# Performance work log

Measured on AMD Instinct MI355X. Metric: run time of the kernel, lower is better.

Reference implementation:

```python
import jax, jax.numpy as jnp
import numpy as np


def ray_sampler(cam2world, intrinsics, resolution):
    # EG3D RaySampler: pixel centers in [0,1], lifted through intrinsics, rotated to world.
    B = cam2world.shape[0]
    fx = intrinsics[:, 0, 0][:, None]
    fy = intrinsics[:, 1, 1][:, None]
    cx = intrinsics[:, 0, 2][:, None]
    cy = intrinsics[:, 1, 2][:, None]
    sk = intrinsics[:, 0, 1][:, None]
    ii, jj = jnp.meshgrid(jnp.arange(resolution), jnp.arange(resolution), indexing='ij')
    # torch.meshgrid + flip(0): x = column index, y = row index (row-major flatten)
    x = ((jj.reshape(-1).astype(jnp.float32) + 0.5) / resolution)[None, :]  # [1, M]
    y = ((ii.reshape(-1).astype(jnp.float32) + 0.5) / resolution)[None, :]  # [1, M]
    x_lift = (x - cx + cy * sk / fy - sk * y / fy) / fx        # [B, M]
    y_lift = (y - cy) / fy                                     # [B, M]
    ones = jnp.ones_like(x_lift)
    cam_rel = jnp.stack([x_lift, y_lift, ones, ones], axis=-1)  # [B, M, 4]
    world = jnp.einsum('bij,bmj->bmi', cam2world, cam_rel)[..., :3]  # [B, M, 3]
    cam_loc = cam2world[:, :3, 3]                               # [B, 3]
    dirs = world - cam_loc[:, None, :]
    dirs = dirs / jnp.maximum(jnp.linalg.norm(dirs, axis=-1, keepdims=True), 1e-12)
    origins = jnp.broadcast_to(cam_loc[:, None, :], dirs.shape)
    return origins, dirs


def setup_inputs() -> dict:
    key = jax.random.key(0)
    k1, k2, k3 = jax.random.split(key, 3)
    B, res, N = 4, 128, 2048
    # realistic camera: identity rotation, camera near z=2.7 (EG3D radius), normalized intrinsics
    t = jnp.concatenate([0.05 * jax.random.normal(k1, (B, 2)), jnp.full((B, 1), 2.7)], axis=1)
    c2w = jnp.tile(jnp.eye(4, dtype=jnp.float32)[None], (B, 1, 1)).at[:, :3, 3].set(t)
    intr = jnp.tile(jnp.array([[4.2647, 0.0, 0.5], [0.0, 4.2647, 0.5], [0.0, 0.0, 1.0]],
                              dtype=jnp.float32)[None], (B, 1, 1))
    c = jnp.concatenate([c2w.reshape(B, 16), intr.reshape(B, 9)], axis=1)  # [B, 25]
    image_depth = 2.2 + jax.random.uniform(k2, (B, 1, res, res), dtype=jnp.float32)
    pc = 0.3 * jax.random.normal(k3, (B, N, 3), dtype=jnp.float32)
    return {"c": c, "image_depth": image_depth, "pc": pc, "neural_rendering_resolution": 128}


def reference(c, image_depth, pc, neural_rendering_resolution):
    B = c.shape[0]
    res = neural_rendering_resolution
    M = res * res
    cam2world = c[:, :16].reshape(B, 4, 4)
    intrinsics = c[:, 16:25].reshape(B, 3, 3)
    ray_origins, ray_dirs = ray_sampler(cam2world, intrinsics, res)  # [B, M, 3] each
    pc3 = pc[..., :3]                                                # [B, N, 3]
    # distance from camera origin to every pc point -> max per sample
    d0 = jnp.linalg.norm(ray_origins[:, :1, :] - pc3, axis=-1)       # [B, N]
    max_distance = jnp.max(d0, axis=1)                               # [B]
    depth = image_depth.reshape(B, M, 1)
    pred = depth * ray_dirs + ray_origins                            # [B, M, 3]
    mask = depth.reshape(B, M) < max_distance[:, None]               # [B, M]
    # chamfer dist1 (direction=0): squared distance of each pred point to nearest pc point
    d2 = (jnp.sum(pred * pred, axis=-1)[:, :, None]
          + jnp.sum(pc3 * pc3, axis=-1)[:, None, :]
          - 2.0 * jnp.einsum('bmd,bnd->bmn', pred, pc3))             # [B, M, N]
    min_d2 = jnp.maximum(jnp.min(d2, axis=2), 0.0)                   # [B, M]
    # ragged masked mean == mean over pred_[mask_] in the original loop
    m = mask.astype(min_d2.dtype)
    loss = jnp.sum(min_d2 * m, axis=1) / jnp.maximum(jnp.sum(m, axis=1), 1.0)
    return loss.reshape(B, 1)
```

## Files before the change

kernel.cpp:

```cpp
#include <hip/hip_runtime.h>
#include <math.h>

#define TPB 512
#define WAVES 8
#define RAYS_PB 256
#define MAXPTS 2048
#define PTILE 32

typedef short short8 __attribute__((ext_vector_type(8)));
typedef float f32x16 __attribute__((ext_vector_type(16)));

__device__ __forceinline__ unsigned int f2bf(float f) {
    unsigned int u = __float_as_uint(f);
    u += 0x7FFFu + ((u >> 16) & 1u);
    return u >> 16;
}

__global__ __launch_bounds__(TPB) void chamfer_main(
    const float* __restrict__ c, const float* __restrict__ depth,
    const float* __restrict__ pc, float2* __restrict__ partial,
    int res, int M, int N)
{
    __shared__ uint2 spts[MAXPTS];
    __shared__ float redR[WAVES][32][33];
    __shared__ float pnL[RAYS_PB], depL[RAYS_PB];
    __shared__ float smax[WAVES];
    __shared__ float bs[4], bc[4];

    int tile = blockIdx.x, b = blockIdx.y;
    int tid = threadIdx.x, w = tid >> 6, lane = tid & 63;
    int colb = lane & 31, hh = lane >> 5;

    const float* cb = c + b * 25;
    float fx = cb[16], sk = cb[17], cx = cb[18];
    float fy = cb[20], cy = cb[21];
    float ox = cb[3], oy = cb[7], oz = cb[11];

    short8 afrag = {0, 0, 0, 0, 0, 0, 0, 0};
    {
        int m = tile * RAYS_PB + w * 32 + colb;
        int mm = min(m, M - 1);
        int i = mm / res, j = mm - i * res;
        float x = (j + 0.5f) / (float)res;
        float y = (i + 0.5f) / (float)res;
        float xl = (x - cx + cy * sk / fy - sk * y / fy) / fx;
        float yl = (y - cy) / fy;
        float wx = cb[0] * xl + cb[1] * yl + cb[2] + cb[3];
        float wy = cb[4] * xl + cb[5] * yl + cb[6] + cb[7];
        float wz = cb[8] * xl + cb[9] * yl + cb[10] + cb[11];
        float dx = wx - ox, dy = wy - oy, dz = wz - oz;
        float nrm = fmaxf(sqrtf(dx * dx + dy * dy + dz * dz), 1e-12f);
        dx /= nrm; dy /= nrm; dz /= nrm;
        float d = depth[(size_t)b * M + mm];
        float px_ = fmaf(d, dx, ox);
        float py_ = fmaf(d, dy, oy);
        float pz_ = fmaf(d, dz, oz);
        float pn_ = px_ * px_ + py_ * py_ + pz_ * pz_;
        if (hh == 0) {
            pnL[w * 32 + colb] = pn_;
            depL[w * 32 + colb] = d;
            afrag[0] = (short)f2bf(px_);
            afrag[1] = (short)f2bf(py_);
            afrag[2] = (short)f2bf(pz_);
            afrag[3] = (short)0x3F80;
        }
    }

    const f32x16 zacc = {0.f,0.f,0.f,0.f,0.f,0.f,0.f,0.f,
                         0.f,0.f,0.f,0.f,0.f,0.f,0.f,0.f};
    float mx[16];
    #pragma unroll
    for (int r = 0; r < 16; ++r) mx[r] = -3.4e38f;

    float mdl = 0.0f;
    for (int n0 = 0; n0 < N; n0 += MAXPTS) {
        int kc = min(N - n0, MAXPTS);
        int kcp = ((kc + PTILE - 1) / PTILE) * PTILE;
        if (n0) __syncthreads();
        const float* src = pc + ((size_t)b * N + n0) * 3;

        int g4 = kc >> 2;
        const float4* s4 = (const float4*)src;
        for (int g = tid; g < g4; g += TPB) {
            float4 f0 = s4[3 * g], f1 = s4[3 * g + 1], f2 = s4[3 * g + 2];
            float qx0 = f0.x, qy0 = f0.y, qz0 = f0.z;
            float qx1 = f0.w, qy1 = f1.x, qz1 = f1.y;
            float qx2 = f1.z, qy2 = f1.w, qz2 = f2.x;
            float qx3 = f2.y, qy3 = f2.z, qz3 = f2.w;
            float w0 = -0.5f * (qx0*qx0 + qy0*qy0 + qz0*qz0);
            float w1 = -0.5f * (qx1*qx1 + qy1*qy1 + qz1*qz1);
            float w2 = -0.5f * (qx2*qx2 + qy2*qy2 + qz2*qz2);
            float w3 = -0.5f * (qx3*qx3 + qy3*qy3 + qz3*qz3);
            spts[4*g+0] = make_uint2(f2bf(qx0) | (f2bf(qy0) << 16), f2bf(qz0) | (f2bf(w0) << 16));
            spts[4*g+1] = make_uint2(f2bf(qx1) | (f2bf(qy1) << 16), f2bf(qz1) | (f2bf(w1) << 16));
            spts[4*g+2] = make_uint2(f2bf(qx2) | (f2bf(qy2) << 16), f2bf(qz2) | (f2bf(w2) << 16));
            spts[4*g+3] = make_uint2(f2bf(qx3) | (f2bf(qy3) << 16), f2bf(qz3) | (f2bf(w3) << 16));
            float a0 = qx0 - ox, a1 = qy0 - oy, a2 = qz0 - oz;
            float b0 = qx1 - ox, b1 = qy1 - oy, b2 = qz1 - oz;
            float c0 = qx2 - ox, c1 = qy2 - oy, c2 = qz2 - oz;
            float d0 = qx3 - ox, d1 = qy3 - oy, d2 = qz3 - oz;
            mdl = fmaxf(mdl, fmaxf(
                fmaxf(a0*a0 + a1*a1 + a2*a2, b0*b0 + b1*b1 + b2*b2),
                fmaxf(c0*c0 + c1*c1 + c2*c2, d0*d0 + d1*d1 + d2*d2)));
        }
        for (int p = (g4 << 2) + tid; p < kc; p += TPB) {
            float qx = src[3*p], qy = src[3*p+1], qz = src[3*p+2];
            float qn = qx*qx + qy*qy + qz*qz;
            spts[p] = make_uint2(f2bf(qx) | (f2bf(qy) << 16),
                                 f2bf(qz) | (f2bf(-0.5f * qn) << 16));
            float dx = qx - ox, dy = qy - oy, dz = qz - oz;
            mdl = fmaxf(mdl, dx*dx + dy*dy + dz*dz);
        }
        for (int p = kc + tid; p < kcp; p += TPB)
            spts[p] = make_uint2(0u, 0xC61C0000u);
        __syncthreads();

        int ntt = kcp >> 5;
        #pragma unroll 2
        for (int t = 0; t < ntt; ++t) {
            uint2 qv = spts[t * 32 + colb];
            union { uint4 u; short8 s; } bu;
            bu.u = make_uint4(qv.x, qv.y, 0u, 0u);
            f32x16 dacc = __builtin_amdgcn_mfma_f32_32x32x16_bf16(
                afrag, bu.s, zacc, 0, 0, 0);
            #pragma unroll
            for (int r = 0; r < 16; ++r) mx[r] = fmaxf(mx[r], dacc[r]);
        }
    }

    for (int off = 32; off; off >>= 1) mdl = fmaxf(mdl, __shfl_down(mdl, off));
    if (lane == 0) smax[w] = mdl;
    #pragma unroll
    for (int r = 0; r < 16; ++r) {
        int row = (r & 3) + 8 * (r >> 2) + 4 * hh;
        redR[w][row][colb] = mx[r];
    }
    __syncthreads();

    float s = 0.f, cnt = 0.f;
    if (tid < RAYS_PB) {
        float m2 = smax[0];
        #pragma unroll
        for (int ww = 1; ww < WAVES; ++ww) m2 = fmaxf(m2, smax[ww]);
        float thr = sqrtf(m2);

        int w2 = tid >> 5, row = tid & 31;
        float mxx = redR[w2][row][0];
        #pragma unroll
        for (int col = 1; col < 32; ++col) mxx = fmaxf(mxx, redR[w2][row][col]);

        int mray = tile * RAYS_PB + tid;
        if (mray < M) {
            float md = fmaxf(fmaf(-2.0f, mxx, pnL[tid]), 0.0f);
            if (depL[tid] < thr) { s = md; cnt = 1.0f; }
        }
    }
    for (int off = 32; off; off >>= 1) {
        s += __shfl_down(s, off);
        cnt += __shfl_down(cnt, off);
    }
    if (tid < RAYS_PB && lane == 0) { bs[w] = s; bc[w] = cnt; }
    __syncthreads();
    if (tid == 0) {
        float S = 0.f, C = 0.f;
        #pragma unroll
        for (int ww = 0; ww < 4; ++ww) { S += bs[ww]; C += bc[ww]; }
        partial[(size_t)b * gridDim.x + blockIdx.x] = make_float2(S, C);
    }
}

__global__ __launch_bounds__(1024) void finalize_kernel(
    const float2* __restrict__ partial, float* __restrict__ out,
    int ntiles, int B)
{
    int w = threadIdx.x >> 6, lane = threadIdx.x & 63;
    if (w >= B) return;
    float S = 0.f, C = 0.f;
    for (int i = lane; i < ntiles; i += 64) {
        float2 p = partial[(size_t)w * ntiles + i];
        S += p.x; C += p.y;
    }
    for (int off = 32; off; off >>= 1) {
        S += __shfl_down(S, off);
        C += __shfl_down(C, off);
    }
    if (lane == 0) out[w] = S / fmaxf(C, 1.0f);
}

extern "C" void kernel_launch(void* const* d_in, const int* in_sizes, int n_in,
                              void* d_out, int out_size, void* d_ws, size_t ws_size,
                              hipStream_t stream) {
    const float* c     = (const float*)d_in[0];
    const float* depth = (const float*)d_in[1];
    const float* pc    = (const float*)d_in[2];

    int B = in_sizes[0] / 25;
    int M = in_sizes[1] / B;
    int N = in_sizes[2] / (3 * B);
    int res = 1;
    while (res * res < M) ++res;

    float2* partial = (float2*)d_ws;
    int ntiles = (M + RAYS_PB - 1) / RAYS_PB;

    chamfer_main<<<dim3(ntiles, B), TPB, 0, stream>>>(c, depth, pc, partial,
                                                      res, M, N);
    finalize_kernel<<<1, B * 64, 0, stream>>>(partial, (float*)d_out,
                                              ntiles, B);
}
```

Baseline: 23.11 us.

## Precompute packed bf16 points in a prep kernel and split point range across waves

Adds a prep kernel that converts each batch's point cloud to packed bf16 (x,y,z,-|q|^2/2) once, writes it to global workspace, and computes per-chunk max camera distances. The main kernel no longer stages every point into LDS per block. It reads the packed points straight from global/L2, halves rays per block to 128, and has two waves split the point range per 32-ray group, merging in the reduction. This removes the redundant per-block conversion and LDS fill and doubles the block count, at the cost of an extra kernel launch and uncoalesced-ish global loads in the MFMA loop.

```diff
diff --git a/kernel.cpp b/kernel.cpp
--- a/kernel.cpp
+++ b/kernel.cpp
@@ -3,9 +3,9 @@
 
 #define TPB 512
 #define WAVES 8
-#define RAYS_PB 256
-#define MAXPTS 2048
-#define PTILE 32
+#define RAYS_PB 128
+#define PREP_BLK 16
+#define PREP_T 128
 
 typedef short short8 __attribute__((ext_vector_type(8)));
 typedef float f32x16 __attribute__((ext_vector_type(16)));
@@ -16,29 +16,65 @@
     return u >> 16;
 }
 
+__global__ __launch_bounds__(PREP_T) void prep_kernel(
+    const float* __restrict__ c, const float* __restrict__ pc,
+    uint2* __restrict__ pts2, float* __restrict__ gpart, int N)
+{
+    int b = blockIdx.y, blk = blockIdx.x;
+    const float* cb = c + b * 25;
+    float ox = cb[3], oy = cb[7], oz = cb[11];
+    const float* p = pc + (size_t)b * N * 3;
+    int per = (N + PREP_BLK - 1) / PREP_BLK;
+    int n0 = blk * per;
+    int n1 = min(n0 + per, N);
+    float mx = 0.0f;
+    for (int n = n0 + threadIdx.x; n < n1; n += PREP_T) {
+        float qx = p[n * 3], qy = p[n * 3 + 1], qz = p[n * 3 + 2];
+        float qn = qx * qx + qy * qy + qz * qz;
+        pts2[(size_t)b * N + n] = make_uint2(
+            f2bf(qx) | (f2bf(qy) << 16),
+            f2bf(qz) | (f2bf(-0.5f * qn) << 16));
+        float dx = qx - ox, dy = qy - oy, dz = qz - oz;
+        mx = fmaxf(mx, dx * dx + dy * dy + dz * dz);
+    }
+    for (int off = 32; off; off >>= 1) mx = fmaxf(mx, __shfl_down(mx, off));
+    __shared__ float sm[PREP_T / 64];
+    if ((threadIdx.x & 63) == 0) sm[threadIdx.x >> 6] = mx;
+    __syncthreads();
+    if (threadIdx.x == 0) {
+        float m2 = sm[0];
+        for (int i = 1; i < PREP_T / 64; ++i) m2 = fmaxf(m2, sm[i]);
+        gpart[b * PREP_BLK + blk] = m2;
+    }
+}
+
 __global__ __launch_bounds__(TPB) void chamfer_main(
     const float* __restrict__ c, const float* __restrict__ depth,
-    const float* __restrict__ pc, float2* __restrict__ partial,
-    int res, int M, int N)
+    const uint2* __restrict__ pts2, const float* __restrict__ gpart,
+    float2* __restrict__ partial, int res, int M, int N)
 {
-    __shared__ uint2 spts[MAXPTS];
     __shared__ float redR[WAVES][32][33];
     __shared__ float pnL[RAYS_PB], depL[RAYS_PB];
-    __shared__ float smax[WAVES];
-    __shared__ float bs[4], bc[4];
+    __shared__ float bs[2], bc[2];
 
     int tile = blockIdx.x, b = blockIdx.y;
     int tid = threadIdx.x, w = tid >> 6, lane = tid & 63;
     int colb = lane & 31, hh = lane >> 5;
+    int rg = w >> 1, half = w & 1;
 
     const float* cb = c + b * 25;
     float fx = cb[16], sk = cb[17], cx = cb[18];
     float fy = cb[20], cy = cb[21];
     float ox = cb[3], oy = cb[7], oz = cb[11];
 
+    float m2 = 0.0f;
+    #pragma unroll
+    for (int i = 0; i < PREP_BLK; ++i) m2 = fmaxf(m2, gpart[b * PREP_BLK + i]);
+    float thr = sqrtf(m2);
+
     short8 afrag = {0, 0, 0, 0, 0, 0, 0, 0};
     {
-        int m = tile * RAYS_PB + w * 32 + colb;
+        int m = tile * RAYS_PB + rg * 32 + colb;
         int mm = min(m, M - 1);
         int i = mm / res, j = mm - i * res;
         float x = (j + 0.5f) / (float)res;
@@ -57,12 +93,14 @@
         float pz_ = fmaf(d, dz, oz);
         float pn_ = px_ * px_ + py_ * py_ + pz_ * pz_;
         if (hh == 0) {
-            pnL[w * 32 + colb] = pn_;
-            depL[w * 32 + colb] = d;
             afrag[0] = (short)f2bf(px_);
             afrag[1] = (short)f2bf(py_);
             afrag[2] = (short)f2bf(pz_);
             afrag[3] = (short)0x3F80;
+            if (half == 0) {
+                pnL[rg * 32 + colb] = pn_;
+                depL[rg * 32 + colb] = d;
+            }
         }
     }
 
@@ -72,64 +110,24 @@
     #pragma unroll
     for (int r = 0; r < 16; ++r) mx[r] = -3.4e38f;
 
-    float mdl = 0.0f;
-    for (int n0 = 0; n0 < N; n0 += MAXPTS) {
-        int kc = min(N - n0, MAXPTS);
-        int kcp = ((kc + PTILE - 1) / PTILE) * PTILE;
-        if (n0) __syncthreads();
-        const float* src = pc + ((size_t)b * N + n0) * 3;
-
-        int g4 = kc >> 2;
-        const float4* s4 = (const float4*)src;
-        for (int g = tid; g < g4; g += TPB) {
-            float4 f0 = s4[3 * g], f1 = s4[3 * g + 1], f2 = s4[3 * g + 2];
-            float qx0 = f0.x, qy0 = f0.y, qz0 = f0.z;
-            float qx1 = f0.w, qy1 = f1.x, qz1 = f1.y;
-            float qx2 = f1.z, qy2 = f1.w, qz2 = f2.x;
-            float qx3 = f2.y, qy3 = f2.z, qz3 = f2.w;
-            float w0 = -0.5f * (qx0*qx0 + qy0*qy0 + qz0*qz0);
-            float w1 = -0.5f * (qx1*qx1 + qy1*qy1 + qz1*qz1);
-            float w2 = -0.5f * (qx2*qx2 + qy2*qy2 + qz2*qz2);
-            float w3 = -0.5f * (qx3*qx3 + qy3*qy3 + qz3*qz3);
-            spts[4*g+0] = make_uint2(f2bf(qx0) | (f2bf(qy0) << 16), f2bf(qz0) | (f2bf(w0) << 16));
-            spts[4*g+1] = make_uint2(f2bf(qx1) | (f2bf(qy1) << 16), f2bf(qz1) | (f2bf(w1) << 16));
-            spts[4*g+2] = make_uint2(f2bf(qx2) | (f2bf(qy2) << 16), f2bf(qz2) | (f2bf(w2) << 16));
-            spts[4*g+3] = make_uint2(f2bf(qx3) | (f2bf(qy3) << 16), f2bf(qz3) | (f2bf(w3) << 16));
-            float a0 = qx0 - ox, a1 = qy0 - oy, a2 = qz0 - oz;
-            float b0 = qx1 - ox, b1 = qy1 - oy, b2 = qz1 - oz;
-            float c0 = qx2 - ox, c1 = qy2 - oy, c2 = qz2 - oz;
-            float d0 = qx3 - ox, d1 = qy3 - oy, d2 = qz3 - oz;
-            mdl = fmaxf(mdl, fmaxf(
-                fmaxf(a0*a0 + a1*a1 + a2*a2, b0*b0 + b1*b1 + b2*b2),
-                fmaxf(c0*c0 + c1*c1 + c2*c2, d0*d0 + d1*d1 + d2*d2)));
-        }
-        for (int p = (g4 << 2) + tid; p < kc; p += TPB) {
-            float qx = src[3*p], qy = src[3*p+1], qz = src[3*p+2];
-            float qn = qx*qx + qy*qy + qz*qz;
-            spts[p] = make_uint2(f2bf(qx) | (f2bf(qy) << 16),
-                                 f2bf(qz) | (f2bf(-0.5f * qn) << 16));
-            float dx = qx - ox, dy = qy - oy, dz = qz - oz;
-            mdl = fmaxf(mdl, dx*dx + dy*dy + dz*dz);
-        }
-        for (int p = kc + tid; p < kcp; p += TPB)
-            spts[p] = make_uint2(0u, 0xC61C0000u);
-        __syncthreads();
-
-        int ntt = kcp >> 5;
-        #pragma unroll 2
-        for (int t = 0; t < ntt; ++t) {
-            uint2 qv = spts[t * 32 + colb];
-            union { uint4 u; short8 s; } bu;
-            bu.u = make_uint4(qv.x, qv.y, 0u, 0u);
-            f32x16 dacc = __builtin_amdgcn_mfma_f32_32x32x16_bf16(
-                afrag, bu.s, zacc, 0, 0, 0);
-            #pragma unroll
-            for (int r = 0; r < 16; ++r) mx[r] = fmaxf(mx[r], dacc[r]);
-        }
-    }
-
-    for (int off = 32; off; off >>= 1) mdl = fmaxf(mdl, __shfl_down(mdl, off));
-    if (lane == 0) smax[w] = mdl;
+    int ntt = (N + 31) >> 5;
+    int nh = (ntt + 1) >> 1;
+    int t0 = half * nh;
+    int t1 = min(ntt, t0 + nh);
+    const uint2* pq = pts2 + (size_t)b * N;
+
+    #pragma unroll 8
+    for (int t = t0; t < t1; ++t) {
+        int idx = min(t * 32 + colb, N - 1);
+        uint2 qv = pq[idx];
+        union { uint4 u; short8 s; } bu;
+        bu.u = make_uint4(qv.x, qv.y, 0u, 0u);
+        f32x16 dacc = __builtin_amdgcn_mfma_f32_32x32x16_bf16(
+            afrag, bu.s, zacc, 0, 0, 0);
+        #pragma unroll
+        for (int r = 0; r < 16; ++r) mx[r] = fmaxf(mx[r], dacc[r]);
+    }
+
     #pragma unroll
     for (int r = 0; r < 16; ++r) {
         int row = (r & 3) + 8 * (r >> 2) + 4 * hh;
@@ -139,16 +137,12 @@
 
     float s = 0.f, cnt = 0.f;
     if (tid < RAYS_PB) {
-        float m2 = smax[0];
+        int rg2 = tid >> 5, row = tid & 31;
+        float mxx = -3.4e38f;
         #pragma unroll
-        for (int ww = 1; ww < WAVES; ++ww) m2 = fmaxf(m2, smax[ww]);
-        float thr = sqrtf(m2);
-
-        int w2 = tid >> 5, row = tid & 31;
-        float mxx = redR[w2][row][0];
-        #pragma unroll
-        for (int col = 1; col < 32; ++col) mxx = fmaxf(mxx, redR[w2][row][col]);
-
+        for (int col = 0; col < 32; ++col)
+            mxx = fmaxf(mxx, fmaxf(redR[2 * rg2][row][col],
+                                   redR[2 * rg2 + 1][row][col]));
         int mray = tile * RAYS_PB + tid;
         if (mray < M) {
             float md = fmaxf(fmaf(-2.0f, mxx, pnL[tid]), 0.0f);
@@ -162,9 +156,7 @@
     if (tid < RAYS_PB && lane == 0) { bs[w] = s; bc[w] = cnt; }
     __syncthreads();
     if (tid == 0) {
-        float S = 0.f, C = 0.f;
-        #pragma unroll
-        for (int ww = 0; ww < 4; ++ww) { S += bs[ww]; C += bc[ww]; }
+        float S = bs[0] + bs[1], C = bc[0] + bc[1];
         partial[(size_t)b * gridDim.x + blockIdx.x] = make_float2(S, C);
     }
 }
@@ -200,11 +192,20 @@
     int res = 1;
     while (res * res < M) ++res;
 
-    float2* partial = (float2*)d_ws;
+    char* base = (char*)d_ws;
+    uint2* pts2 = (uint2*)base;
+    size_t o = (size_t)B * N * sizeof(uint2);
+    o = (o + 255) & ~(size_t)255;
+    float* gpart = (float*)(base + o);
+    o += (size_t)B * PREP_BLK * sizeof(float);
+    o = (o + 255) & ~(size_t)255;
+    float2* partial = (float2*)(base + o);
+
     int ntiles = (M + RAYS_PB - 1) / RAYS_PB;
 
-    chamfer_main<<<dim3(ntiles, B), TPB, 0, stream>>>(c, depth, pc, partial,
-                                                      res, M, N);
+    prep_kernel<<<dim3(PREP_BLK, B), PREP_T, 0, stream>>>(c, pc, pts2, gpart, N);
+    chamfer_main<<<dim3(ntiles, B), TPB, 0, stream>>>(c, depth, pts2, gpart,
+                                                      partial, res, M, N);
     finalize_kernel<<<1, B * 64, 0, stream>>>(partial, (float*)d_out,
                                               ntiles, B);
 }
```

Measured after the change: 29.97 us. +29.7%, slower.
